# Performance work log

Hardware: AMD Instinct MI355X
Metric: run time of the kernel (lower is better)

The kernel has to match this reference:

```python
import jax, jax.numpy as jnp
import numpy as np

NUM_CLASSES = 19
K = 100                 # max_views_per_class
TEMP = 0.1
BASE_TEMP = 0.07
EPS_NORM = 1e-12


def _l2_normalize(x):
    # matches torch F.normalize(dim=1): x / max(||x||, eps)
    n = jnp.sqrt(jnp.sum(x * x, axis=1, keepdims=True))
    return x / jnp.maximum(n, EPS_NORM)


def _sample_indices(labels_flat):
    # Deterministic per-class sampler: first K pixels of each class.
    # (torch version uses randperm; the downstream math is identical.)
    # Every class is guaranteed >= K pixels by input construction.
    idxs = [jnp.where(labels_flat == c, size=K, fill_value=0)[0]
            for c in range(NUM_CLASSES)]
    return jnp.concatenate(idxs)  # [NUM_CLASSES*K]


def setup_inputs() -> dict:
    key = jax.random.key(0)
    k1, k2, k3, k4 = jax.random.split(key, 4)
    pixel_feats = jax.random.normal(k1, (8, 256, 128, 128), dtype=jnp.float32)
    labels = jax.random.randint(k2, (8, 128, 128), 0, NUM_CLASSES).astype(jnp.int64)
    memory_feats = jax.random.normal(k3, (20000, 256), dtype=jnp.float32)
    memory_labels = jax.random.randint(k4, (20000,), 0, NUM_CLASSES).astype(jnp.int64)
    return {"pixel_feats": pixel_feats, "labels": labels,
            "memory_feats": memory_feats, "memory_labels": memory_labels}


def reference(pixel_feats, labels, memory_feats, memory_labels):
    B, D, H, W = pixel_feats.shape
    feats_flat = pixel_feats.transpose(0, 2, 3, 1).reshape(-1, D)   # [B*H*W, D]
    labels_flat = labels.reshape(-1)

    idx = _sample_indices(labels_flat)
    anchor_feats = feats_flat[idx]                                  # [Na, D]
    anchor_labels = jnp.repeat(jnp.arange(NUM_CLASSES), K)          # [Na]

    contrast_feats = jnp.concatenate([anchor_feats, memory_feats], axis=0)
    contrast_labels = jnp.concatenate([anchor_labels, memory_labels], axis=0)

    a = _l2_normalize(anchor_feats)
    c = _l2_normalize(contrast_feats)
    logits = jnp.einsum('nd,md->nm', a, c) / TEMP                   # [Na, Nc]

    Na, Nc = logits.shape
    mask = (anchor_labels[:, None] == contrast_labels[None, :]).astype(logits.dtype)
    # remove self-contrast (diagonal of the first Na contrast columns)
    rows = jnp.arange(Na)
    logits_mask = jnp.ones((Na, Nc), dtype=logits.dtype).at[rows, rows].set(0.0)
    mask = mask * logits_mask

    exp_logits = jnp.exp(logits) * logits_mask
    log_prob = logits - jnp.log(exp_logits.sum(axis=1, keepdims=True) + 1e-12)

    pos_count = mask.sum(axis=1)                                    # [Na]
    valid = pos_count > 0
    mean_log_prob_pos = (mask * log_prob).sum(axis=1) / jnp.maximum(pos_count, 1.0)
    n_valid = jnp.maximum(jnp.sum(valid).astype(logits.dtype), 1.0)
    loss = -(TEMP / BASE_TEMP) * (jnp.sum(jnp.where(valid, mean_log_prob_pos, 0.0)) / n_valid)
    return loss
```

## Files before the change

kernel.cpp:

```cpp
#include <hip/hip_runtime.h>
#include <hip/hip_bf16.h>
#include <math.h>

#define NCLS   19
#define KPC    100
#define NA     1900
#define NM     20000
#define NC     21900
#define NCP2   22016
#define D      256
#define HW     16384
#define NPIX   131072
#define NT_M   15
#define NT_N   172
#define NTILES (NT_M * NT_N)

#define B_SAMPLE 0
#define B_MEM    19
#define B_CLAB   2519
#define B_PAD    2605
#define B_ZERO   2620
#define K1_GRID  2621

typedef __attribute__((ext_vector_type(8))) short bf16x8;
typedef __attribute__((ext_vector_type(4))) float f32x4;

#define WS_ROWS  64
#define WS_ROWP  7744
#define WS_IDX   15424
#define WS_CLAB  30720
#define WS_CT2   118784

__device__ __forceinline__ short f2bf(float x) {
    __hip_bfloat16 h = __float2bfloat16(x);
    return *(short*)&h;
}

__global__ void prep_kernel(const int* __restrict__ labels, const float* __restrict__ mem,
                            const int* __restrict__ memlab,
                            int* __restrict__ idx, int* __restrict__ clab,
                            short* __restrict__ Ct2,
                            float* __restrict__ rowS, float* __restrict__ rowP) {
    const int b = blockIdx.x;
    const int t = threadIdx.x;
    if (b < B_MEM) {
        const int c = b;
        const int wave = t >> 6, lane = t & 63;
        __shared__ int s_base;
        __shared__ int s_wavecnt[4];
        if (t == 0) s_base = 0;
        __syncthreads();
        for (int start = 0; start < NPIX; start += 256) {
            const int i = start + t;
            const bool pred = (labels[i] == c);
            const unsigned long long bm = __ballot(pred);
            if (lane == 0) s_wavecnt[wave] = __popcll(bm);
            __syncthreads();
            const int base = s_base;
            int wbase = 0;
            for (int w = 0; w < wave; ++w) wbase += s_wavecnt[w];
            const int chunk_total = s_wavecnt[0] + s_wavecnt[1] + s_wavecnt[2] + s_wavecnt[3];
            if (pred) {
                const int rank = base + wbase + __popcll(bm & ((1ULL << lane) - 1ULL));
                if (rank < KPC) idx[c * KPC + rank] = i;
            }
            __syncthreads();
            if (t == 0) s_base = base + chunk_total;
            if (base + chunk_total >= KPC) break;
        }
    } else if (b < B_CLAB) {
        const int r  = (b - B_MEM) * 8 + (t >> 5);
        const int kq = t & 31;
        const float4 v0 = *(const float4*)(mem + (size_t)r * D + kq * 8);
        const float4 v1 = *(const float4*)(mem + (size_t)r * D + kq * 8 + 4);
        float ssq = v0.x*v0.x + v0.y*v0.y + v0.z*v0.z + v0.w*v0.w
                  + v1.x*v1.x + v1.y*v1.y + v1.z*v1.z + v1.w*v1.w;
        #pragma unroll
        for (int o = 16; o; o >>= 1) ssq += __shfl_xor(ssq, o, 32);
        const float inv = 1.0f / fmaxf(sqrtf(ssq), 1e-12f);
        bf16x8 ov;
        ov[0] = f2bf(v0.x * inv); ov[1] = f2bf(v0.y * inv);
        ov[2] = f2bf(v0.z * inv); ov[3] = f2bf(v0.w * inv);
        ov[4] = f2bf(v1.x * inv); ov[5] = f2bf(v1.y * inv);
        ov[6] = f2bf(v1.z * inv); ov[7] = f2bf(v1.w * inv);
        *(bf16x8*)(Ct2 + ((size_t)kq * NCP2 + NA + r) * 8) = ov;
    } else if (b < B_PAD) {
        const int i = (b - B_CLAB) * 256 + t;
        clab[i] = (i < NA) ? ((i * 5243) >> 19)
                           : ((i < NC) ? memlab[i - NA] : -1);
    } else if (b < B_ZERO) {
        const int e = (b - B_PAD) * 256 + t;
        if (e < 32 * (NCP2 - NC)) {
            const int kq = e / (NCP2 - NC);
            const int n  = NC + (e - kq * (NCP2 - NC));
            bf16x8 z = {};
            *(bf16x8*)(Ct2 + ((size_t)kq * NCP2 + n) * 8) = z;
        }
    } else {
        for (int i = t; i < 1920; i += 256) { rowS[i] = 0.f; rowP[i] = 0.f; }
    }
}

__global__ void anchor_kernel(const float* __restrict__ pixel, const int* __restrict__ idx,
                              short* __restrict__ Ct2) {
    const int t = threadIdx.x;
    const int a = blockIdx.x * 8 + (t >> 5);
    const int kq = t & 31;
    if (a >= NA) return;
    const int p = idx[a];
    const int bi = p >> 14;
    const int hw = p & (HW - 1);
    const float* base = pixel + ((size_t)(bi * D + kq * 8)) * HW + hw;
    float v[8];
    float ssq = 0.f;
    #pragma unroll
    for (int j = 0; j < 8; ++j) { v[j] = base[(size_t)j * HW]; ssq += v[j] * v[j]; }
    #pragma unroll
    for (int o = 16; o; o >>= 1) ssq += __shfl_xor(ssq, o, 32);
    const float inv = 1.0f / fmaxf(sqrtf(ssq), 1e-12f);
    bf16x8 ov;
    #pragma unroll
    for (int j = 0; j < 8; ++j) ov[j] = f2bf(v[j] * inv);
    *(bf16x8*)(Ct2 + ((size_t)kq * NCP2 + a) * 8) = ov;
}

__global__ __launch_bounds__(256, 4)
void mfma_gemm_kernel(const short* __restrict__ Ct2, const int* __restrict__ clab,
                      float* __restrict__ rowS, float* __restrict__ rowP) {
    __shared__ int s_nlab[128];
    const int tid  = threadIdx.x;
    const int lane = tid & 63;
    const int w    = tid >> 6;
    const int wm   = w >> 1, wn = w & 1;
    const int quad = lane >> 4;
    const int l16  = lane & 15;

    const int bid = blockIdx.x;
    const int x   = bid & 7;
    const int j   = bid >> 3;
    const int wg  = (x < 4 ? x * 323 : 1292 + (x - 4) * 322) + j;
    const int m0  = (wg % NT_M) * 128;
    const int n0  = (wg / NT_M) * 128;

    if (tid < 128) s_nlab[tid] = clab[n0 + tid];

    const int aCol = m0 + wm * 64 + l16;
    const int bCol = n0 + wn * 64 + l16;

    f32x4 acc[4][4] = {};

    #pragma unroll
    for (int kb = 0; kb < 8; ++kb) {
        const int kqb = kb * 4 + quad;
        const short* kbase = Ct2 + (size_t)kqb * NCP2 * 8;
        bf16x8 af[4], bfr[4];
        #pragma unroll
        for (int mi = 0; mi < 4; ++mi)
            af[mi] = *(const bf16x8*)(kbase + (size_t)(aCol + mi * 16) * 8);
        #pragma unroll
        for (int ni = 0; ni < 4; ++ni)
            bfr[ni] = *(const bf16x8*)(kbase + (size_t)(bCol + ni * 16) * 8);
        #pragma unroll
        for (int ni = 0; ni < 4; ++ni)
            #pragma unroll
            for (int mi = 0; mi < 4; ++mi)
                acc[ni][mi] = __builtin_amdgcn_mfma_f32_16x16x32_bf16(
                    bfr[ni], af[mi], acc[ni][mi], 0, 0, 0);
    }

    __syncthreads();

    const int m_base = m0 + wm * 64 + l16;
    #pragma unroll
    for (int mi = 0; mi < 4; ++mi) {
        const int m    = m_base + mi * 16;
        const int mlab = (m * 5243) >> 19;
        float s = 0.f, p = 0.f;
        #pragma unroll
        for (int ni = 0; ni < 4; ++ni) {
            const int nb = wn * 64 + ni * 16 + quad * 4;
            const int4 lb = *(const int4*)&s_nlab[nb];
            #pragma unroll
            for (int r = 0; r < 4; ++r) {
                const int n  = n0 + nb + r;
                const int nl = (&lb.x)[r];
                if (n < NC && n != m) {
                    const float l = acc[ni][mi][r] * 10.0f;
                    s += __expf(l);
                    if (nl == mlab) p += l;
                }
            }
        }
        s += __shfl_xor(s, 16, 64); s += __shfl_xor(s, 32, 64);
        p += __shfl_xor(p, 16, 64); p += __shfl_xor(p, 32, 64);
        if (quad == 0 && m < NA) {
            atomicAdd(&rowS[m], s);
            atomicAdd(&rowP[m], p);
        }
    }
}

__global__ void finalize_kernel(const float* __restrict__ rowS, const float* __restrict__ rowP,
                                const int* __restrict__ memlab, float* __restrict__ out) {
    const int t = threadIdx.x;
    __shared__ int hist[NCLS];
    __shared__ float rs[4], rn[4];
    if (t < NCLS) hist[t] = 0;
    __syncthreads();
    for (int i = t; i < NM; i += 256) atomicAdd(&hist[memlab[i]], 1);
    __syncthreads();
    float sum = 0.f, nval = 0.f;
    for (int n = t; n < NA; n += 256) {
        const float cnt  = (float)(KPC - 1 + hist[(n * 5243) >> 19]);
        const float logS = logf(rowS[n] + 1e-12f);
        const float mean = (rowP[n] - cnt * logS) / fmaxf(cnt, 1.0f);
        if (cnt > 0.f) { sum += mean; nval += 1.f; }
    }
    for (int o = 32; o; o >>= 1) {
        sum  += __shfl_xor(sum, o, 64);
        nval += __shfl_xor(nval, o, 64);
    }
    if ((t & 63) == 0) { rs[t >> 6] = sum; rn[t >> 6] = nval; }
    __syncthreads();
    if (t == 0) {
        const float s  = rs[0] + rs[1] + rs[2] + rs[3];
        const float nv = rn[0] + rn[1] + rn[2] + rn[3];
        out[0] = -(0.1f / 0.07f) * (s / fmaxf(nv, 1.f));
    }
}

extern "C" void kernel_launch(void* const* d_in, const int* in_sizes, int n_in,
                              void* d_out, int out_size, void* d_ws, size_t ws_size,
                              hipStream_t stream) {
    const float* pixel  = (const float*)d_in[0];
    const int*   labels = (const int*)d_in[1];
    const float* mem    = (const float*)d_in[2];
    const int*   memlab = (const int*)d_in[3];
    char* ws = (char*)d_ws;
    float* rowS = (float*)(ws + WS_ROWS);
    float* rowP = (float*)(ws + WS_ROWP);
    int*   idx  = (int*)(ws + WS_IDX);
    int*   clab = (int*)(ws + WS_CLAB);
    short* Ct2  = (short*)(ws + WS_CT2);
    float* out  = (float*)d_out;

    prep_kernel<<<dim3(K1_GRID), dim3(256), 0, stream>>>(
        labels, mem, memlab, idx, clab, Ct2, rowS, rowP);
    anchor_kernel<<<dim3(238), dim3(256), 0, stream>>>(pixel, idx, Ct2);
    mfma_gemm_kernel<<<dim3(NTILES), dim3(256), 0, stream>>>(Ct2, clab, rowS, rowP);
    finalize_kernel<<<dim3(1), dim3(256), 0, stream>>>(rowS, rowP, memlab, out);
}
```

Measured before the change: 242.7 us.

## Fuse anchor gather into prep kernel and vectorize memlab histogram

Each class's sampling is split across 13 blocks. Every block rescans the labels up to its own rank window, then gathers and normalizes its 8 anchor rows in place. This removes the separate anchor_kernel launch and the idx round-trip through global memory. The cost is that the label scan is repeated roughly 13 times per class. The finalize histogram now reads memlab as int4 vectors.

```diff
diff --git a/kernel.cpp b/kernel.cpp
--- a/kernel.cpp
+++ b/kernel.cpp
@@ -15,19 +15,19 @@
 #define NT_N   172
 #define NTILES (NT_M * NT_N)
 
-#define B_SAMPLE 0
-#define B_MEM    19
-#define B_CLAB   2519
-#define B_PAD    2605
-#define B_ZERO   2620
-#define K1_GRID  2621
+#define ABPC    13
+#define B_ANCH  0
+#define B_MEM   247
+#define B_CLAB  2747
+#define B_PAD   2833
+#define B_ZERO  2848
+#define K1_GRID 2849
 
 typedef __attribute__((ext_vector_type(8))) short bf16x8;
 typedef __attribute__((ext_vector_type(4))) float f32x4;
 
 #define WS_ROWS  64
 #define WS_ROWP  7744
-#define WS_IDX   15424
 #define WS_CLAB  30720
 #define WS_CT2   118784
 
@@ -36,16 +36,18 @@
     return *(short*)&h;
 }
 
-__global__ void prep_kernel(const int* __restrict__ labels, const float* __restrict__ mem,
-                            const int* __restrict__ memlab,
-                            int* __restrict__ idx, int* __restrict__ clab,
-                            short* __restrict__ Ct2,
+__global__ void prep_kernel(const float* __restrict__ pixel, const int* __restrict__ labels,
+                            const float* __restrict__ mem, const int* __restrict__ memlab,
+                            int* __restrict__ clab, short* __restrict__ Ct2,
                             float* __restrict__ rowS, float* __restrict__ rowP) {
     const int b = blockIdx.x;
     const int t = threadIdx.x;
     if (b < B_MEM) {
-        const int c = b;
+        const int c    = b / ABPC;
+        const int r0   = (b % ABPC) * 8;
+        const int rmax = (r0 + 8 < KPC) ? r0 + 8 : KPC;
         const int wave = t >> 6, lane = t & 63;
+        __shared__ int s_idx[8];
         __shared__ int s_base;
         __shared__ int s_wavecnt[4];
         if (t == 0) s_base = 0;
@@ -62,11 +64,33 @@
             const int chunk_total = s_wavecnt[0] + s_wavecnt[1] + s_wavecnt[2] + s_wavecnt[3];
             if (pred) {
                 const int rank = base + wbase + __popcll(bm & ((1ULL << lane) - 1ULL));
-                if (rank < KPC) idx[c * KPC + rank] = i;
+                if (rank >= r0 && rank < rmax) s_idx[rank - r0] = i;
             }
             __syncthreads();
             if (t == 0) s_base = base + chunk_total;
-            if (base + chunk_total >= KPC) break;
+            if (base + chunk_total >= rmax) break;
+        }
+        __syncthreads();
+        const int ai = t >> 5;
+        const int kq = t & 31;
+        const int r  = r0 + ai;
+        if (r < rmax) {
+            const int a   = c * KPC + r;
+            const int pix = s_idx[ai];
+            const int bi  = pix >> 14;
+            const int hw  = pix & (HW - 1);
+            const float* base = pixel + ((size_t)(bi * D + kq * 8)) * HW + hw;
+            float v[8];
+            float ssq = 0.f;
+            #pragma unroll
+            for (int j = 0; j < 8; ++j) { v[j] = base[(size_t)j * HW]; ssq += v[j] * v[j]; }
+            #pragma unroll
+            for (int o = 16; o; o >>= 1) ssq += __shfl_xor(ssq, o, 32);
+            const float inv = 1.0f / fmaxf(sqrtf(ssq), 1e-12f);
+            bf16x8 ov;
+            #pragma unroll
+            for (int j = 0; j < 8; ++j) ov[j] = f2bf(v[j] * inv);
+            *(bf16x8*)(Ct2 + ((size_t)kq * NCP2 + a) * 8) = ov;
         }
     } else if (b < B_CLAB) {
         const int r  = (b - B_MEM) * 8 + (t >> 5);
@@ -101,29 +125,6 @@
     }
 }
 
-__global__ void anchor_kernel(const float* __restrict__ pixel, const int* __restrict__ idx,
-                              short* __restrict__ Ct2) {
-    const int t = threadIdx.x;
-    const int a = blockIdx.x * 8 + (t >> 5);
-    const int kq = t & 31;
-    if (a >= NA) return;
-    const int p = idx[a];
-    const int bi = p >> 14;
-    const int hw = p & (HW - 1);
-    const float* base = pixel + ((size_t)(bi * D + kq * 8)) * HW + hw;
-    float v[8];
-    float ssq = 0.f;
-    #pragma unroll
-    for (int j = 0; j < 8; ++j) { v[j] = base[(size_t)j * HW]; ssq += v[j] * v[j]; }
-    #pragma unroll
-    for (int o = 16; o; o >>= 1) ssq += __shfl_xor(ssq, o, 32);
-    const float inv = 1.0f / fmaxf(sqrtf(ssq), 1e-12f);
-    bf16x8 ov;
-    #pragma unroll
-    for (int j = 0; j < 8; ++j) ov[j] = f2bf(v[j] * inv);
-    *(bf16x8*)(Ct2 + ((size_t)kq * NCP2 + a) * 8) = ov;
-}
-
 __global__ __launch_bounds__(256, 4)
 void mfma_gemm_kernel(const short* __restrict__ Ct2, const int* __restrict__ clab,
                       float* __restrict__ rowS, float* __restrict__ rowP) {
@@ -207,7 +208,13 @@
     __shared__ float rs[4], rn[4];
     if (t < NCLS) hist[t] = 0;
     __syncthreads();
-    for (int i = t; i < NM; i += 256) atomicAdd(&hist[memlab[i]], 1);
+    for (int i4 = t; i4 < NM / 4; i4 += 256) {
+        const int4 v = ((const int4*)memlab)[i4];
+        atomicAdd(&hist[v.x], 1);
+        atomicAdd(&hist[v.y], 1);
+        atomicAdd(&hist[v.z], 1);
+        atomicAdd(&hist[v.w], 1);
+    }
     __syncthreads();
     float sum = 0.f, nval = 0.f;
     for (int n = t; n < NA; n += 256) {
@@ -239,14 +246,12 @@
     char* ws = (char*)d_ws;
     float* rowS = (float*)(ws + WS_ROWS);
     float* rowP = (float*)(ws + WS_ROWP);
-    int*   idx  = (int*)(ws + WS_IDX);
     int*   clab = (int*)(ws + WS_CLAB);
     short* Ct2  = (short*)(ws + WS_CT2);
     float* out  = (float*)d_out;
 
     prep_kernel<<<dim3(K1_GRID), dim3(256), 0, stream>>>(
-        labels, mem, memlab, idx, clab, Ct2, rowS, rowP);
-    anchor_kernel<<<dim3(238), dim3(256), 0, stream>>>(pixel, idx, Ct2);
+        pixel, labels, mem, memlab, clab, Ct2, rowS, rowP);
     mfma_gemm_kernel<<<dim3(NTILES), dim3(256), 0, stream>>>(Ct2, clab, rowS, rowP);
     finalize_kernel<<<dim3(1), dim3(256), 0, stream>>>(rowS, rowP, memlab, out);
 }
```

Result: faster. 230.4 us (-5.1%).
